# Kernel optimization log

Measured on AMD Instinct MI355X. Metric: run time of the kernel, lower is better.

## Reference

```python
import jax, jax.numpy as jnp
import numpy as np

NEG_SLOPE = 0.2

def setup_inputs() -> dict:
    key = jax.random.key(0)
    k1, k2, k3, k4, k5 = jax.random.split(key, 5)
    B, N, Fin, Fout, H = 4, 2048, 256, 128, 4
    h = jax.random.normal(k1, (B, N, Fin), dtype=jnp.float32)
    adj = jax.random.randint(k2, (N, N), 0, 2, dtype=jnp.int32)
    W_w = jax.random.normal(k3, (Fout, Fin), dtype=jnp.float32) * (1.414 / np.sqrt(Fin))
    W_b = jax.random.normal(k4, (Fout,), dtype=jnp.float32) * 0.01
    attn_w = jax.random.normal(k5, (H, 2 * Fout), dtype=jnp.float32) * (1.414 / np.sqrt(2 * Fout))
    return {"h": h, "adj": adj, "W_w": W_w, "W_b": W_b, "attn_w": attn_w}

def reference(h, adj, W_w, W_b, attn_w):
    Fout = W_w.shape[0]
    # Wh: [B, N, Fout]
    Wh = jnp.einsum('bnf,of->bno', h, W_w) + W_b
    a_left = attn_w[:, :Fout]   # [H, Fout]
    a_right = attn_w[:, Fout:]  # [H, Fout]
    e_left = jnp.einsum('bno,ho->bhn', Wh, a_left)   # [B, H, N]
    e_right = jnp.einsum('bno,ho->bhn', Wh, a_right)  # [B, H, N]
    # additive broadcast score: [B, H, N, N]
    e = e_left[:, :, :, None] + e_right[:, :, None, :]
    e = jnp.where(e > 0, e, NEG_SLOPE * e)  # LeakyReLU(0.2)
    mask = (adj == 0)[None, None, :, :]     # [1,1,N,N] broadcast over B,H
    e = jnp.where(mask, -jnp.inf, e)
    attn = jax.nn.softmax(e, axis=-1)
    attn = jnp.where(jnp.isnan(attn), 0.0, attn)
    # h_prime: [B, H, N, Fout]
    h_prime = jnp.einsum('bhij,bjo->bhio', attn, Wh)
    out = jnp.mean(h_prime, axis=1)
    return jax.nn.relu(out)
```

## Files before the change

kernel.cpp:

```cpp
#include <hip/hip_runtime.h>
#include <stdint.h>

#define BB 4
#define NN 2048
#define FIN 256
#define FOUT 128
#define NH 4
#define NEG_SLOPE 0.2f

typedef short bf16x8 __attribute__((ext_vector_type(8)));
typedef unsigned short u16x8 __attribute__((ext_vector_type(8)));
typedef float f32x4 __attribute__((ext_vector_type(4)));
typedef unsigned long long u64;

__device__ inline float b2f(unsigned short u) {
    union { unsigned int i; float f; } x; x.i = ((unsigned int)u) << 16; return x.f;
}
__device__ inline unsigned short f2b(float f) {
    union { float f; unsigned int i; } x; x.f = f;
    unsigned int r = x.i + 0x7fffu + ((x.i >> 16) & 1u);
    return (unsigned short)(r >> 16);
}
__device__ inline unsigned short f2b_fast(float f) {
    union { float f; unsigned int i; } x; x.f = f;
    return (unsigned short)((x.i + 0x8000u) >> 16);
}


__global__ __launch_bounds__(256) void k0_prep(const float* __restrict__ Ww,
                                               unsigned short* __restrict__ Whi,
                                               unsigned short* __restrict__ Wlo,
                                               const int* __restrict__ adj,
                                               u64* __restrict__ mask) {
    int bid = blockIdx.x;
    if (bid < 128) {
        int idx = bid * 256 + threadIdx.x;
        float v = Ww[idx];
        unsigned short hb = f2b(v);
        Whi[idx] = hb;
        Wlo[idx] = f2b(v - b2f(hb));
    } else {
        int row = bid - 128;
        int wave = threadIdx.x >> 6, lane = threadIdx.x & 63;
        #pragma unroll
        for (int it = 0; it < 8; ++it) {
            int w = it * 4 + wave;
            int j = w * 64 + lane;
            u64 m = __ballot(adj[(size_t)row * NN + j] != 0);
            if (lane == 0) mask[row * 32 + w] = m;
        }
    }
}

__global__ __launch_bounds__(256) void k1_wh(
    const float* __restrict__ h, const unsigned short* __restrict__ Whi,
    const unsigned short* __restrict__ Wlo, const float* __restrict__ Wb,
    const float* __restrict__ attw, unsigned short* __restrict__ WhT,
    float2* __restrict__ ELpair, float2* __restrict__ ERf) {
    __shared__ unsigned short Ahi[16][264];
    __shared__ unsigned short Alo[16][264];
    __shared__ float whs[16][132];
    int t = threadIdx.x;
    int b = blockIdx.x >> 7;
    int n0 = (blockIdx.x & 127) * 16;
    {
        int r = t >> 4, c = (t & 15) * 16;
        const float* hp = h + ((size_t)(b * NN + n0 + r)) * FIN + c;
        u16x8 hi0, hi1, lo0, lo1;
        #pragma unroll
        for (int q = 0; q < 4; ++q) {
            float4 v = *(const float4*)(hp + q * 4);
            float vv[4] = {v.x, v.y, v.z, v.w};
            #pragma unroll
            for (int e = 0; e < 4; ++e) {
                int idx = q * 4 + e;
                unsigned short hb = f2b(vv[e]);
                unsigned short lb = f2b(vv[e] - b2f(hb));
                if (idx < 8) { hi0[idx] = (short)hb; lo0[idx] = (short)lb; }
                else         { hi1[idx - 8] = (short)hb; lo1[idx - 8] = (short)lb; }
            }
        }
        *(u16x8*)&Ahi[r][c] = *(u16x8*)&hi0;
        *(u16x8*)&Ahi[r][c + 8] = *(u16x8*)&hi1;
        *(u16x8*)&Alo[r][c] = *(u16x8*)&lo0;
        *(u16x8*)&Alo[r][c + 8] = *(u16x8*)&lo1;
    }
    __syncthreads();
    int lane = t & 63, wv = t >> 6;
    int m = lane & 15, quad = lane >> 4;
    int o0 = wv * 32;
    f32x4 acc0 = {0.f, 0.f, 0.f, 0.f}, acc1 = {0.f, 0.f, 0.f, 0.f};
    const unsigned short* wh0 = Whi + (size_t)(o0 + m) * FIN;
    const unsigned short* wl0 = Wlo + (size_t)(o0 + m) * FIN;
    const unsigned short* wh1 = Whi + (size_t)(o0 + 16 + m) * FIN;
    const unsigned short* wl1 = Wlo + (size_t)(o0 + 16 + m) * FIN;
    #pragma unroll
    for (int ks = 0; ks < 8; ++ks) {
        int ko = ks * 32 + quad * 8;
        bf16x8 ahi = *(bf16x8*)&Ahi[m][ko];
        bf16x8 alo = *(bf16x8*)&Alo[m][ko];
        bf16x8 bh0 = *(const bf16x8*)(wh0 + ko);
        bf16x8 bl0 = *(const bf16x8*)(wl0 + ko);
        bf16x8 bh1 = *(const bf16x8*)(wh1 + ko);
        bf16x8 bl1 = *(const bf16x8*)(wl1 + ko);
        acc0 = __builtin_amdgcn_mfma_f32_16x16x32_bf16(ahi, bh0, acc0, 0, 0, 0);
        acc0 = __builtin_amdgcn_mfma_f32_16x16x32_bf16(ahi, bl0, acc0, 0, 0, 0);
        acc0 = __builtin_amdgcn_mfma_f32_16x16x32_bf16(alo, bh0, acc0, 0, 0, 0);
        acc1 = __builtin_amdgcn_mfma_f32_16x16x32_bf16(ahi, bh1, acc1, 0, 0, 0);
        acc1 = __builtin_amdgcn_mfma_f32_16x16x32_bf16(ahi, bl1, acc1, 0, 0, 0);
        acc1 = __builtin_amdgcn_mfma_f32_16x16x32_bf16(alo, bh1, acc1, 0, 0, 0);
    }
    float bias0 = Wb[o0 + m], bias1 = Wb[o0 + 16 + m];
    #pragma unroll
    for (int reg = 0; reg < 4; ++reg) {
        int row = quad * 4 + reg;
        whs[row][o0 + m] = acc0[reg] + bias0;
        whs[row][o0 + 16 + m] = acc1[reg] + bias1;
    }
    __syncthreads();
    {
        int o = t >> 1, half = t & 1;
        u16x8 v8;
        #pragma unroll
        for (int r = 0; r < 8; ++r) v8[r] = (short)f2b(whs[half * 8 + r][o]);
        *(u16x8*)(WhT + (size_t)(b * FOUT + o) * NN + n0 + half * 8) = v8;
    }
    {
        int outi = t >> 1, half = t & 1;
        int i = outi >> 3, d = outi & 7, hh = d & 3, side = d >> 2;
        const float* arow = attw + hh * (2 * FOUT) + side * FOUT + half * 64;
        float s = 0.f;
        #pragma unroll 8
        for (int k = 0; k < 64; ++k) s = fmaf(whs[i][half * 64 + k], arow[k], s);
        s += __shfl_xor(s, 1);
        if (half == 0) {
            float p = __expf(s), n = __expf(NEG_SLOPE * s);
            if (side == 0) {
                ELpair[(size_t)(b * NH + hh) * NN + n0 + i] = make_float2(p, n);
            } else {
                ERf[((size_t)b * NN + n0 + i) * NH + hh] = make_float2(p, n);
            }
        }
    }
}

__global__ __launch_bounds__(512, 2) void k2_reg(
    const unsigned short* __restrict__ WhT, const float2* __restrict__ ERf,
    const float2* __restrict__ ELpair, const u64* __restrict__ mask,
    float* __restrict__ out) {
    __shared__ char smem[65536 + 8448 + 1024];
    float4* erf4 = (float4*)smem;
    u64* mlds = (u64*)(smem + 65536);
    float* sred = (float*)(smem + 65536 + 8448);
    int t = threadIdx.x;
    int b = blockIdx.y, i0 = blockIdx.x * 32;
    int lane = t & 63, wv = t >> 6;
    int m = lane & 15, quad = lane >> 4;
    int isub = wv & 1, oq = (wv >> 1) & 1, kp = wv >> 2;

    {
        const float4* src = (const float4*)(ERf + (size_t)b * NN * NH);
        #pragma unroll
        for (int i = 0; i < 8; ++i) erf4[t + i * 512] = src[t + i * 512];
    }
    {
        #pragma unroll
        for (int i = 0; i < 2; ++i) {
            int idx = t + i * 512;
            int r = idx >> 5, w = idx & 31;
            mlds[r * 33 + w] = mask[(size_t)(i0 + r) * 32 + w];
        }
    }
    int irow = i0 + isub * 16 + m;
    float elp[NH], eln[NH];
    #pragma unroll
    for (int hh = 0; hh < NH; ++hh) {
        float2 e2 = ELpair[(size_t)(b * NH + hh) * NN + irow];
        elp[hh] = e2.x; eln[hh] = e2.y;
    }
    __syncthreads();

    bf16x8 ones;
    #pragma unroll
    for (int e = 0; e < 8; ++e) ones[e] = (short)0x3F80;

    const unsigned short* bp0 = WhT + (size_t)(b * FOUT + oq * 64 +  0 + m) * NN;
    const unsigned short* bp1 = WhT + (size_t)(b * FOUT + oq * 64 + 16 + m) * NN;
    const unsigned short* bp2 = WhT + (size_t)(b * FOUT + oq * 64 + 32 + m) * NN;
    const unsigned short* bp3 = WhT + (size_t)(b * FOUT + oq * 64 + 48 + m) * NN;

    f32x4 acc[4][4];
    f32x4 sacc[4];
    #pragma unroll
    for (int f = 0; f < 4; ++f)
        #pragma unroll
        for (int hh = 0; hh < NH; ++hh) acc[f][hh] = (f32x4){0.f, 0.f, 0.f, 0.f};
    #pragma unroll
    for (int hh = 0; hh < NH; ++hh) sacc[hh] = (f32x4){0.f, 0.f, 0.f, 0.f};

    int mr = isub * 16 + m;

    for (int it = 0; it < 32; ++it) {
        int ks = (it << 1) | kp;
        int jb = ks * 32 + quad * 8;
        bf16x8 bfr0 = *(const bf16x8*)(bp0 + jb);
        bf16x8 bfr1 = *(const bf16x8*)(bp1 + jb);
        bf16x8 bfr2 = *(const bf16x8*)(bp2 + jb);
        bf16x8 bfr3 = *(const bf16x8*)(bp3 + jb);
        u64 w64 = mlds[mr * 33 + (ks >> 1)];
        unsigned mb = (unsigned)(w64 >> (((ks & 1) << 5) + (quad << 3))) & 0xFFu;
        bf16x8 af0, af1, af2, af3;
        #pragma unroll
        for (int e = 0; e < 8; ++e) {
            float4 e0 = erf4[(jb + e) * 2];
            float4 e1 = erf4[(jb + e) * 2 + 1];
            bool bit = (mb >> e) & 1u;
            float w0 = fmaxf(elp[0] * e0.x, eln[0] * e0.y);
            float w1 = fmaxf(elp[1] * e0.z, eln[1] * e0.w);
            float w2 = fmaxf(elp[2] * e1.x, eln[2] * e1.y);
            float w3 = fmaxf(elp[3] * e1.z, eln[3] * e1.w);
            af0[e] = bit ? (short)f2b_fast(w0) : (short)0;
            af1[e] = bit ? (short)f2b_fast(w1) : (short)0;
            af2[e] = bit ? (short)f2b_fast(w2) : (short)0;
            af3[e] = bit ? (short)f2b_fast(w3) : (short)0;
        }
        sacc[0] = __builtin_amdgcn_mfma_f32_16x16x32_bf16(af0, ones, sacc[0], 0, 0, 0);
        sacc[1] = __builtin_amdgcn_mfma_f32_16x16x32_bf16(af1, ones, sacc[1], 0, 0, 0);
        sacc[2] = __builtin_amdgcn_mfma_f32_16x16x32_bf16(af2, ones, sacc[2], 0, 0, 0);
        sacc[3] = __builtin_amdgcn_mfma_f32_16x16x32_bf16(af3, ones, sacc[3], 0, 0, 0);
        acc[0][0] = __builtin_amdgcn_mfma_f32_16x16x32_bf16(af0, bfr0, acc[0][0], 0, 0, 0);
        acc[0][1] = __builtin_amdgcn_mfma_f32_16x16x32_bf16(af1, bfr0, acc[0][1], 0, 0, 0);
        acc[0][2] = __builtin_amdgcn_mfma_f32_16x16x32_bf16(af2, bfr0, acc[0][2], 0, 0, 0);
        acc[0][3] = __builtin_amdgcn_mfma_f32_16x16x32_bf16(af3, bfr0, acc[0][3], 0, 0, 0);
        acc[1][0] = __builtin_amdgcn_mfma_f32_16x16x32_bf16(af0, bfr1, acc[1][0], 0, 0, 0);
        acc[1][1] = __builtin_amdgcn_mfma_f32_16x16x32_bf16(af1, bfr1, acc[1][1], 0, 0, 0);
        acc[1][2] = __builtin_amdgcn_mfma_f32_16x16x32_bf16(af2, bfr1, acc[1][2], 0, 0, 0);
        acc[1][3] = __builtin_amdgcn_mfma_f32_16x16x32_bf16(af3, bfr1, acc[1][3], 0, 0, 0);
        acc[2][0] = __builtin_amdgcn_mfma_f32_16x16x32_bf16(af0, bfr2, acc[2][0], 0, 0, 0);
        acc[2][1] = __builtin_amdgcn_mfma_f32_16x16x32_bf16(af1, bfr2, acc[2][1], 0, 0, 0);
        acc[2][2] = __builtin_amdgcn_mfma_f32_16x16x32_bf16(af2, bfr2, acc[2][2], 0, 0, 0);
        acc[2][3] = __builtin_amdgcn_mfma_f32_16x16x32_bf16(af3, bfr2, acc[2][3], 0, 0, 0);
        acc[3][0] = __builtin_amdgcn_mfma_f32_16x16x32_bf16(af0, bfr3, acc[3][0], 0, 0, 0);
        acc[3][1] = __builtin_amdgcn_mfma_f32_16x16x32_bf16(af1, bfr3, acc[3][1], 0, 0, 0);
        acc[3][2] = __builtin_amdgcn_mfma_f32_16x16x32_bf16(af2, bfr3, acc[3][2], 0, 0, 0);
        acc[3][3] = __builtin_amdgcn_mfma_f32_16x16x32_bf16(af3, bfr3, acc[3][3], 0, 0, 0);
    }
    __syncthreads();

    float* cred = (float*)smem;
    int p = wv & 3;
    if (kp == 1) {
        #pragma unroll
        for (int f = 0; f < 4; ++f)
            #pragma unroll
            for (int hh = 0; hh < NH; ++hh)
                #pragma unroll
                for (int r = 0; r < 4; ++r)
                    cred[(((p * 4 + f) * 4 + hh) * 4 + r) * 64 + lane] = acc[f][hh][r];
        if (m == 0) {
            #pragma unroll
            for (int hh = 0; hh < NH; ++hh)
                #pragma unroll
                for (int r = 0; r < 4; ++r)
                    sred[((p * 4 + hh) * 4 + r) * 4 + quad] = sacc[hh][r];
        }
    }
    __syncthreads();
    if (kp == 0) {
        #pragma unroll
        for (int r = 0; r < 4; ++r) {
            float inv[NH];
            #pragma unroll
            for (int hh = 0; hh < NH; ++hh) {
                float S = sacc[hh][r] + sred[((p * 4 + hh) * 4 + r) * 4 + quad];
                inv[hh] = (S > 0.f) ? 1.f / S : 0.f;
            }
            int orow = i0 + isub * 16 + quad * 4 + r;
            #pragma unroll
            for (int f = 0; f < 4; ++f) {
                float v = 0.f;
                #pragma unroll
                for (int hh = 0; hh < NH; ++hh)
                    v += (acc[f][hh][r] +
                          cred[(((p * 4 + f) * 4 + hh) * 4 + r) * 64 + lane]) * inv[hh];
                out[((size_t)b * NN + orow) * FOUT + oq * 64 + f * 16 + m] =
                    fmaxf(0.25f * v, 0.f);
            }
        }
    }
}

extern "C" void kernel_launch(void* const* d_in, const int* in_sizes, int n_in,
                              void* d_out, int out_size, void* d_ws, size_t ws_size,
                              hipStream_t stream) {
    const float* h    = (const float*)d_in[0];
    const int* adj    = (const int*)d_in[1];
    const float* Ww   = (const float*)d_in[2];
    const float* Wb   = (const float*)d_in[3];
    const float* attw = (const float*)d_in[4];
    float* out = (float*)d_out;
    char* ws = (char*)d_ws;
    unsigned short* Whi = (unsigned short*)(ws);
    unsigned short* Wlo = (unsigned short*)(ws + 65536);
    unsigned short* WhT = (unsigned short*)(ws + 131072);
    float2*       ELpair = (float2*)(ws + 2228224);
    float2*       ERf    = (float2*)(ws + 2490368);
    u64*          mask   = (u64*)(ws + 2752512);

    k0_prep<<<dim3(128 + NN), dim3(256), 0, stream>>>(Ww, Whi, Wlo, adj, mask);
    k1_wh<<<dim3(BB * NN / 16), dim3(256), 0, stream>>>(h, Whi, Wlo, Wb, attw,
                                                        WhT, ELpair, ERf);
    k2_reg<<<dim3(NN / 32, BB), dim3(512), 0, stream>>>(WhT, ERf, ELpair,
                                                        mask, out);
}
```

Baseline: 128.5 us.

## Widen k2 waves to all 128 outputs, split K four ways, swizzle ERf LDS

```diff
diff --git a/kernel.cpp b/kernel.cpp
--- a/kernel.cpp
+++ b/kernel.cpp
@@ -29,34 +29,32 @@
 
 __global__ __launch_bounds__(256) void k0_prep(const float* __restrict__ Ww,
                                                unsigned short* __restrict__ Whi,
-                                               unsigned short* __restrict__ Wlo,
-                                               const int* __restrict__ adj,
-                                               u64* __restrict__ mask) {
-    int bid = blockIdx.x;
-    if (bid < 128) {
-        int idx = bid * 256 + threadIdx.x;
-        float v = Ww[idx];
-        unsigned short hb = f2b(v);
-        Whi[idx] = hb;
-        Wlo[idx] = f2b(v - b2f(hb));
-    } else {
-        int row = bid - 128;
-        int wave = threadIdx.x >> 6, lane = threadIdx.x & 63;
-        #pragma unroll
-        for (int it = 0; it < 8; ++it) {
-            int w = it * 4 + wave;
-            int j = w * 64 + lane;
-            u64 m = __ballot(adj[(size_t)row * NN + j] != 0);
-            if (lane == 0) mask[row * 32 + w] = m;
-        }
-    }
+                                               unsigned short* __restrict__ Wlo) {
+    int idx = blockIdx.x * 256 + threadIdx.x;
+    float v = Ww[idx];
+    unsigned short hb = f2b(v);
+    Whi[idx] = hb;
+    Wlo[idx] = f2b(v - b2f(hb));
 }
 
 __global__ __launch_bounds__(256) void k1_wh(
     const float* __restrict__ h, const unsigned short* __restrict__ Whi,
     const unsigned short* __restrict__ Wlo, const float* __restrict__ Wb,
     const float* __restrict__ attw, unsigned short* __restrict__ WhT,
-    float2* __restrict__ ELpair, float2* __restrict__ ERf) {
+    float2* __restrict__ ELpair, float2* __restrict__ ERf,
+    const int* __restrict__ adj, u64* __restrict__ mask) {
+    if (blockIdx.x >= BB * NN / 16) {
+        int row = blockIdx.x - BB * NN / 16;
+        int wave = threadIdx.x >> 6, lane = threadIdx.x & 63;
+        #pragma unroll
+        for (int it = 0; it < 8; ++it) {
+            int w = it * 4 + wave;
+            int j = w * 64 + lane;
+            u64 mm = __ballot(adj[(size_t)row * NN + j] != 0);
+            if (lane == 0) mask[row * 32 + w] = mm;
+        }
+        return;
+    }
     __shared__ unsigned short Ahi[16][264];
     __shared__ unsigned short Alo[16][264];
     __shared__ float whs[16][132];
@@ -148,20 +146,23 @@
     const unsigned short* __restrict__ WhT, const float2* __restrict__ ERf,
     const float2* __restrict__ ELpair, const u64* __restrict__ mask,
     float* __restrict__ out) {
-    __shared__ char smem[65536 + 8448 + 1024];
+    __shared__ char smem[65600 + 8448 + 1536];
     float4* erf4 = (float4*)smem;
-    u64* mlds = (u64*)(smem + 65536);
-    float* sred = (float*)(smem + 65536 + 8448);
+    u64* mlds = (u64*)(smem + 65600);
+    float* sred = (float*)(smem + 65600 + 8448);
     int t = threadIdx.x;
     int b = blockIdx.y, i0 = blockIdx.x * 32;
     int lane = t & 63, wv = t >> 6;
     int m = lane & 15, quad = lane >> 4;
-    int isub = wv & 1, oq = (wv >> 1) & 1, kp = wv >> 2;
+    int isub = wv & 1, kp = wv >> 1;
 
     {
         const float4* src = (const float4*)(ERf + (size_t)b * NN * NH);
         #pragma unroll
-        for (int i = 0; i < 8; ++i) erf4[t + i * 512] = src[t + i * 512];
+        for (int i = 0; i < 8; ++i) {
+            int g = t + i * 512;
+            erf4[g ^ (((g >> 4) & 3) << 1)] = src[g];
+        }
     }
     {
         #pragma unroll
@@ -184,36 +185,38 @@
     #pragma unroll
     for (int e = 0; e < 8; ++e) ones[e] = (short)0x3F80;
 
-    const unsigned short* bp0 = WhT + (size_t)(b * FOUT + oq * 64 +  0 + m) * NN;
-    const unsigned short* bp1 = WhT + (size_t)(b * FOUT + oq * 64 + 16 + m) * NN;
-    const unsigned short* bp2 = WhT + (size_t)(b * FOUT + oq * 64 + 32 + m) * NN;
-    const unsigned short* bp3 = WhT + (size_t)(b * FOUT + oq * 64 + 48 + m) * NN;
-
-    f32x4 acc[4][4];
-    f32x4 sacc[4];
-    #pragma unroll
-    for (int f = 0; f < 4; ++f)
+    const unsigned short* bp[8];
+    #pragma unroll
+    for (int f = 0; f < 8; ++f)
+        bp[f] = WhT + (size_t)(b * FOUT + f * 16 + m) * NN + kp * 32 + quad * 8;
+
+    f32x4 acc[8][NH];
+    f32x4 sacc[NH];
+    #pragma unroll
+    for (int f = 0; f < 8; ++f)
         #pragma unroll
         for (int hh = 0; hh < NH; ++hh) acc[f][hh] = (f32x4){0.f, 0.f, 0.f, 0.f};
     #pragma unroll
     for (int hh = 0; hh < NH; ++hh) sacc[hh] = (f32x4){0.f, 0.f, 0.f, 0.f};
 
     int mr = isub * 16 + m;
-
-    for (int it = 0; it < 32; ++it) {
-        int ks = (it << 1) | kp;
+    int qs = quad << 1;
+
+    for (int it = 0; it < 16; ++it) {
+        int ks = (it << 2) | kp;
         int jb = ks * 32 + quad * 8;
-        bf16x8 bfr0 = *(const bf16x8*)(bp0 + jb);
-        bf16x8 bfr1 = *(const bf16x8*)(bp1 + jb);
-        bf16x8 bfr2 = *(const bf16x8*)(bp2 + jb);
-        bf16x8 bfr3 = *(const bf16x8*)(bp3 + jb);
+        bf16x8 bfr[8];
+        #pragma unroll
+        for (int f = 0; f < 8; ++f) bfr[f] = *(const bf16x8*)(bp[f]);
         u64 w64 = mlds[mr * 33 + (ks >> 1)];
         unsigned mb = (unsigned)(w64 >> (((ks & 1) << 5) + (quad << 3))) & 0xFFu;
+        int gb = jb * 2;
         bf16x8 af0, af1, af2, af3;
         #pragma unroll
         for (int e = 0; e < 8; ++e) {
-            float4 e0 = erf4[(jb + e) * 2];
-            float4 e1 = erf4[(jb + e) * 2 + 1];
+            int a0 = (gb + e * 2) ^ qs;
+            float4 e0 = erf4[a0];
+            float4 e1 = erf4[a0 + 1];
             bool bit = (mb >> e) & 1u;
             float w0 = fmaxf(elp[0] * e0.x, eln[0] * e0.y);
             float w1 = fmaxf(elp[1] * e0.z, eln[1] * e0.w);
@@ -228,64 +231,72 @@
         sacc[1] = __builtin_amdgcn_mfma_f32_16x16x32_bf16(af1, ones, sacc[1], 0, 0, 0);
         sacc[2] = __builtin_amdgcn_mfma_f32_16x16x32_bf16(af2, ones, sacc[2], 0, 0, 0);
         sacc[3] = __builtin_amdgcn_mfma_f32_16x16x32_bf16(af3, ones, sacc[3], 0, 0, 0);
-        acc[0][0] = __builtin_amdgcn_mfma_f32_16x16x32_bf16(af0, bfr0, acc[0][0], 0, 0, 0);
-        acc[0][1] = __builtin_amdgcn_mfma_f32_16x16x32_bf16(af1, bfr0, acc[0][1], 0, 0, 0);
-        acc[0][2] = __builtin_amdgcn_mfma_f32_16x16x32_bf16(af2, bfr0, acc[0][2], 0, 0, 0);
-        acc[0][3] = __builtin_amdgcn_mfma_f32_16x16x32_bf16(af3, bfr0, acc[0][3], 0, 0, 0);
-        acc[1][0] = __builtin_amdgcn_mfma_f32_16x16x32_bf16(af0, bfr1, acc[1][0], 0, 0, 0);
-        acc[1][1] = __builtin_amdgcn_mfma_f32_16x16x32_bf16(af1, bfr1, acc[1][1], 0, 0, 0);
-        acc[1][2] = __builtin_amdgcn_mfma_f32_16x16x32_bf16(af2, bfr1, acc[1][2], 0, 0, 0);
-        acc[1][3] = __builtin_amdgcn_mfma_f32_16x16x32_bf16(af3, bfr1, acc[1][3], 0, 0, 0);
-        acc[2][0] = __builtin_amdgcn_mfma_f32_16x16x32_bf16(af0, bfr2, acc[2][0], 0, 0, 0);
-        acc[2][1] = __builtin_amdgcn_mfma_f32_16x16x32_bf16(af1, bfr2, acc[2][1], 0, 0, 0);
-        acc[2][2] = __builtin_amdgcn_mfma_f32_16x16x32_bf16(af2, bfr2, acc[2][2], 0, 0, 0);
-        acc[2][3] = __builtin_amdgcn_mfma_f32_16x16x32_bf16(af3, bfr2, acc[2][3], 0, 0, 0);
-        acc[3][0] = __builtin_amdgcn_mfma_f32_16x16x32_bf16(af0, bfr3, acc[3][0], 0, 0, 0);
-        acc[3][1] = __builtin_amdgcn_mfma_f32_16x16x32_bf16(af1, bfr3, acc[3][1], 0, 0, 0);
-        acc[3][2] = __builtin_amdgcn_mfma_f32_16x16x32_bf16(af2, bfr3, acc[3][2], 0, 0, 0);
-        acc[3][3] = __builtin_amdgcn_mfma_f32_16x16x32_bf16(af3, bfr3, acc[3][3], 0, 0, 0);
+        #pragma unroll
+        for (int f = 0; f < 8; ++f) {
+            acc[f][0] = __builtin_amdgcn_mfma_f32_16x16x32_bf16(af0, bfr[f], acc[f][0], 0, 0, 0);
+            acc[f][1] = __builtin_amdgcn_mfma_f32_16x16x32_bf16(af1, bfr[f], acc[f][1], 0, 0, 0);
+            acc[f][2] = __builtin_amdgcn_mfma_f32_16x16x32_bf16(af2, bfr[f], acc[f][2], 0, 0, 0);
+            acc[f][3] = __builtin_amdgcn_mfma_f32_16x16x32_bf16(af3, bfr[f], acc[f][3], 0, 0, 0);
+        }
+        #pragma unroll
+        for (int f = 0; f < 8; ++f) bp[f] += 128;
     }
     __syncthreads();
 
-    float* cred = (float*)smem;
-    int p = wv & 3;
-    if (kp == 1) {
-        #pragma unroll
-        for (int f = 0; f < 4; ++f)
-            #pragma unroll
-            for (int hh = 0; hh < NH; ++hh)
+    float* red = (float*)smem;
+    if (kp && m == 0) {
+        #pragma unroll
+        for (int hh = 0; hh < NH; ++hh)
+            #pragma unroll
+            for (int r = 0; r < 4; ++r)
+                sred[(((kp - 1) * 2 + isub) * 16 + hh * 4 + r) * 4 + quad] = sacc[hh][r];
+    }
+    float v[8][4], inv[4][4];
+    #pragma unroll
+    for (int hh = 0; hh < NH; ++hh) {
+        if (kp) {
+            #pragma unroll
+            for (int f = 0; f < 8; ++f)
                 #pragma unroll
                 for (int r = 0; r < 4; ++r)
-                    cred[(((p * 4 + f) * 4 + hh) * 4 + r) * 64 + lane] = acc[f][hh][r];
-        if (m == 0) {
-            #pragma unroll
-            for (int hh = 0; hh < NH; ++hh)
+                    red[((((kp - 1) * 2 + isub) * 8 + f) * 4 + r) * 64 + lane] = acc[f][hh][r];
+        }
+        __syncthreads();
+        if (kp == 0) {
+            if (hh == 0) {
                 #pragma unroll
-                for (int r = 0; r < 4; ++r)
-                    sred[((p * 4 + hh) * 4 + r) * 4 + quad] = sacc[hh][r];
-        }
-    }
-    __syncthreads();
+                for (int h2 = 0; h2 < NH; ++h2)
+                    #pragma unroll
+                    for (int r = 0; r < 4; ++r) {
+                        float S = sacc[h2][r];
+                        #pragma unroll
+                        for (int k2 = 0; k2 < 3; ++k2)
+                            S += sred[((k2 * 2 + isub) * 16 + h2 * 4 + r) * 4 + quad];
+                        inv[h2][r] = (S > 0.f) ? 1.f / S : 0.f;
+                    }
+            }
+            #pragma unroll
+            for (int f = 0; f < 8; ++f)
+                #pragma unroll
+                for (int r = 0; r < 4; ++r) {
+                    float tot = acc[f][hh][r];
+                    #pragma unroll
+                    for (int k2 = 0; k2 < 3; ++k2)
+                        tot += red[(((k2 * 2 + isub) * 8 + f) * 4 + r) * 64 + lane];
+                    float t2 = tot * inv[hh][r];
+                    if (hh == 0) v[f][r] = t2; else v[f][r] += t2;
+                }
+        }
+        __syncthreads();
+    }
     if (kp == 0) {
         #pragma unroll
         for (int r = 0; r < 4; ++r) {
-            float inv[NH];
-            #pragma unroll
-            for (int hh = 0; hh < NH; ++hh) {
-                float S = sacc[hh][r] + sred[((p * 4 + hh) * 4 + r) * 4 + quad];
-                inv[hh] = (S > 0.f) ? 1.f / S : 0.f;
-            }
             int orow = i0 + isub * 16 + quad * 4 + r;
             #pragma unroll
-            for (int f = 0; f < 4; ++f) {
-                float v = 0.f;
-                #pragma unroll
-                for (int hh = 0; hh < NH; ++hh)
-                    v += (acc[f][hh][r] +
-                          cred[(((p * 4 + f) * 4 + hh) * 4 + r) * 64 + lane]) * inv[hh];
-                out[((size_t)b * NN + orow) * FOUT + oq * 64 + f * 16 + m] =
-                    fmaxf(0.25f * v, 0.f);
-            }
+            for (int f = 0; f < 8; ++f)
+                out[((size_t)b * NN + orow) * FOUT + f * 16 + m] =
+                    fmaxf(0.25f * v[f][r], 0.f);
         }
     }
 }
@@ -307,9 +318,10 @@
     float2*       ERf    = (float2*)(ws + 2490368);
     u64*          mask   = (u64*)(ws + 2752512);
 
-    k0_prep<<<dim3(128 + NN), dim3(256), 0, stream>>>(Ww, Whi, Wlo, adj, mask);
-    k1_wh<<<dim3(BB * NN / 16), dim3(256), 0, stream>>>(h, Whi, Wlo, Wb, attw,
-                                                        WhT, ELpair, ERf);
+    k0_prep<<<dim3(128), dim3(256), 0, stream>>>(Ww, Whi, Wlo);
+    k1_wh<<<dim3(BB * NN / 16 + NN), dim3(256), 0, stream>>>(h, Whi, Wlo, Wb, attw,
+                                                             WhT, ELpair, ERf,
+                                                             adj, mask);
     k2_reg<<<dim3(NN / 32, BB), dim3(512), 0, stream>>>(WhT, ERf, ELpair,
                                                         mask, out);
 }
```

New measurement: 125.4 us (median of 3 runs). 2.4% less time.
